# Kernel tuning notes

Hardware: AMD Instinct MI355X
Metric: run time of the kernel (lower is better)

## Reference

```python
import jax, jax.numpy as jnp
import numpy as np

HIDDEN = 2048
NUM_HEADS = 16
HEAD_SIZE = HIDDEN // NUM_HEADS  # 128
SEQ = 2048
BATCH = 2


def alibi_causal_bias(seq_len: int, num_heads: int) -> jnp.ndarray:
    """[1, H, S, S] bias: -(i-j)*slope for j<=i, -inf for j>i (per source mask)."""
    i = jnp.arange(seq_len)[:, None]
    j = jnp.arange(seq_len)[None, :]
    dist = -(i - j).astype(jnp.float32)            # 0 on diag, -(i-j) below
    causal = jnp.where(j > i, -jnp.inf, 0.0)
    base = jnp.where(j > i, 0.0, dist) + causal     # [S, S]
    if num_heads <= 8:
        slopes = jnp.asarray([1.0 / 2**k for k in range(num_heads)], jnp.float32)
    else:
        slopes = jnp.asarray([1.0 / 2**(k / 2) for k in range(num_heads)], jnp.float32)
    # NOTE: source multiplies the mask (including -inf part) by the slope;
    # -inf * positive slope is still -inf, so applying slopes to the finite
    # part and adding -inf causal term is equivalent.
    return slopes[None, :, None, None] * dist[None, None] * (j <= i)[None, None] + causal[None, None]


def setup_inputs() -> dict:
    key = jax.random.key(0)
    ks = jax.random.split(key, 3)
    sd = 1.0 / np.sqrt(HIDDEN)
    return {
        "x": jax.random.normal(ks[0], (BATCH, SEQ, HIDDEN), jnp.float32),
        "Wqkv": jax.random.normal(ks[1], (HIDDEN, 3 * HIDDEN), jnp.float32) * sd,
        "bqkv": jnp.zeros((3 * HIDDEN,), jnp.float32),
        "Wo": jax.random.normal(ks[2], (HIDDEN, HIDDEN), jnp.float32) * sd,
        "bo": jnp.zeros((HIDDEN,), jnp.float32),
    }


def reference(x, Wqkv, bqkv, Wo, bo):
    b, s, h = x.shape
    scale = 1.0 / np.sqrt(HEAD_SIZE)
    qkv = x @ Wqkv + bqkv                                   # [b, s, 3h]
    q, k, v = jnp.split(qkv, 3, axis=-1)
    def heads(t):
        return t.reshape(b, s, NUM_HEADS, HEAD_SIZE).transpose(0, 2, 1, 3)
    q, k, v = heads(q), heads(k), heads(v)                  # [b, H, s, d]
    scores = jnp.einsum("bhid,bhjd->bhij", q, k) * scale
    scores = scores + alibi_causal_bias(s, NUM_HEADS)
    attn = jax.nn.softmax(scores, axis=-1)                  # dropout=0 (eval)
    out = jnp.einsum("bhij,bhjd->bhid", attn, v)            # [b, H, s, d]
    out = out.transpose(0, 2, 1, 3).reshape(b, s, NUM_HEADS * HEAD_SIZE)
    return out @ Wo + bo
```

## Files before the change

### kernel.cpp

```cpp
#include <hip/hip_runtime.h>

typedef __attribute__((ext_vector_type(4))) float f32x4;
typedef __attribute__((ext_vector_type(8))) __bf16 bf16x8;
typedef unsigned short u16;

#define GAS(p) ((const __attribute__((address_space(1))) void*)(p))
#define LAS(p) ((__attribute__((address_space(3))) void*)(p))

__device__ __forceinline__ u16 f32_to_bf16(float f) {
  unsigned u = __builtin_bit_cast(unsigned, f);
  u += 0x7FFFu + ((u >> 16) & 1u);
  return (u16)(u >> 16);
}

__global__ __launch_bounds__(256) void k_convert(const float* __restrict__ X,
                                                 u16* __restrict__ Y, int n4) {
  int i = blockIdx.x * 256 + threadIdx.x;
  if (i >= n4) return;
  float4 v = ((const float4*)X)[i];
  ushort4 r;
  r.x = f32_to_bf16(v.x); r.y = f32_to_bf16(v.y);
  r.z = f32_to_bf16(v.z); r.w = f32_to_bf16(v.w);
  ((ushort4*)Y)[i] = r;
}

__global__ __launch_bounds__(256) void k_transpose_w(const float* __restrict__ W,
                                                     u16* __restrict__ WT,
                                                     int K, int N) {
  __shared__ float tile[32][33];
  int n0 = blockIdx.x * 32, k0 = blockIdx.y * 32;
  int tx = threadIdx.x & 31, ty = threadIdx.x >> 5;
#pragma unroll
  for (int r = 0; r < 4; ++r)
    tile[ty + r * 8][tx] = W[(long)(k0 + ty + r * 8) * N + n0 + tx];
  __syncthreads();
#pragma unroll
  for (int r = 0; r < 4; ++r)
    WT[(long)(n0 + ty + r * 8) * K + k0 + tx] = f32_to_bf16(tile[tx][ty + r * 8]);
}

__global__ __launch_bounds__(256) void k_transpose_v(const u16* __restrict__ V,
                                                     u16* __restrict__ VT) {
  __shared__ u16 tile[32][34];
  int s0 = blockIdx.x * 32, d0 = blockIdx.y * 32, bh = blockIdx.z;
  int tx = threadIdx.x & 31, ty = threadIdx.x >> 5;
  const u16* Vb = V + (long)bh * 2048 * 128;
  u16* VTb = VT + (long)bh * 128 * 2048;
#pragma unroll
  for (int r = 0; r < 4; ++r)
    tile[ty + r * 8][tx] = Vb[(long)(s0 + ty + r * 8) * 128 + d0 + tx];
  __syncthreads();
#pragma unroll
  for (int r = 0; r < 4; ++r)
    VTb[(long)(d0 + ty + r * 8) * 2048 + s0 + tx] = tile[tx][ty + r * 8];
}

template <int EPI>
__global__ __launch_bounds__(256) void k_gemm(
    const u16* __restrict__ A, const u16* __restrict__ BT,
    const float* __restrict__ bias,
    u16* __restrict__ Qo, u16* __restrict__ Ko, u16* __restrict__ Vo,
    float* __restrict__ Cout, int M, int N, int K) {
  __shared__ alignas(16) u16 As[128 * 32];
  __shared__ alignas(16) u16 Bs[128 * 32];
  const int t = threadIdx.x;
  const int wave = t >> 6, lane = t & 63;
  const int wr = wave >> 1, wc = wave & 1;
  const int l15 = lane & 15, l4 = lane >> 4;
  const int brow = blockIdx.x * 128, bcol = blockIdx.y * 128;

  const f32x4 fzero = {0.f, 0.f, 0.f, 0.f};
  f32x4 acc[4][4];
#pragma unroll
  for (int m = 0; m < 4; ++m)
#pragma unroll
    for (int n = 0; n < 4; ++n) acc[m][n] = fzero;

  const int c0 = wave * 64 + lane;
  const int c1 = 256 + c0;
  const u16* ga0 = A + (long)(brow + (c0 >> 2)) * K + (c0 & 3) * 8;
  const u16* ga1 = A + (long)(brow + (c1 >> 2)) * K + (c1 & 3) * 8;
  const u16* gb0 = BT + (long)(bcol + (c0 >> 2)) * K + (c0 & 3) * 8;
  const u16* gb1 = BT + (long)(bcol + (c1 >> 2)) * K + (c1 & 3) * 8;
  char* lA0 = (char*)As + (wave * 64) * 16;
  char* lA1 = (char*)As + (256 + wave * 64) * 16;
  char* lB0 = (char*)Bs + (wave * 64) * 16;
  char* lB1 = (char*)Bs + (256 + wave * 64) * 16;

  for (int k0 = 0; k0 < K; k0 += 32) {
    __builtin_amdgcn_global_load_lds(GAS(ga0 + k0), LAS(lA0), 16, 0, 0);
    __builtin_amdgcn_global_load_lds(GAS(ga1 + k0), LAS(lA1), 16, 0, 0);
    __builtin_amdgcn_global_load_lds(GAS(gb0 + k0), LAS(lB0), 16, 0, 0);
    __builtin_amdgcn_global_load_lds(GAS(gb1 + k0), LAS(lB1), 16, 0, 0);
    __syncthreads();
    bf16x8 af[4], bf[4];
#pragma unroll
    for (int m = 0; m < 4; ++m)
      af[m] = *(const bf16x8*)(As + (wr * 64 + m * 16 + l15) * 32 + l4 * 8);
#pragma unroll
    for (int n = 0; n < 4; ++n)
      bf[n] = *(const bf16x8*)(Bs + (wc * 64 + n * 16 + l15) * 32 + l4 * 8);
#pragma unroll
    for (int m = 0; m < 4; ++m)
#pragma unroll
      for (int n = 0; n < 4; ++n)
        acc[m][n] =
            __builtin_amdgcn_mfma_f32_16x16x32_bf16(af[m], bf[n], acc[m][n], 0, 0, 0);
    __syncthreads();
  }

  if (EPI == 0) {
    const int which = bcol >> 11;
    u16* dst = (which == 0) ? Qo : (which == 1) ? Ko : Vo;
    const int cbase = bcol & 2047;
#pragma unroll
    for (int n = 0; n < 4; ++n) {
      int col = cbase + wc * 64 + n * 16 + l15;
      int h = col >> 7, d = col & 127;
      float bv = bias[bcol + wc * 64 + n * 16 + l15];
#pragma unroll
      for (int m = 0; m < 4; ++m) {
#pragma unroll
        for (int r = 0; r < 4; ++r) {
          int row = brow + wr * 64 + m * 16 + l4 * 4 + r;
          int b = row >> 11, s = row & 2047;
          dst[(((long)(b * 16 + h)) * 2048 + s) * 128 + d] =
              f32_to_bf16(acc[m][n][r] + bv);
        }
      }
    }
  } else {
#pragma unroll
    for (int m = 0; m < 4; ++m) {
#pragma unroll
      for (int r = 0; r < 4; ++r) {
        int row = brow + wr * 64 + m * 16 + l4 * 4 + r;
#pragma unroll
        for (int n = 0; n < 4; ++n) {
          int col = bcol + wc * 64 + n * 16 + l15;
          Cout[(long)row * N + col] = acc[m][n][r] + bias[col];
        }
      }
    }
  }
}

__global__ __launch_bounds__(256, 4) void k_attn(const u16* __restrict__ Q,
                                                 const u16* __restrict__ Kp,
                                                 const u16* __restrict__ VT,
                                                 u16* __restrict__ Oa) {
  __shared__ alignas(16) u16 Kl[2][64 * 128];
  __shared__ alignas(16) u16 Vl[2][128 * 64];
  __shared__ alignas(16) u16 Pl[4][16 * 64];
  const int b = blockIdx.x;
  const int bh = b & 31;
  const int qt = 31 - (b >> 5);
  const int bb = bh >> 4, h = bh & 15;
  const int wave = threadIdx.x >> 6, lane = threadIdx.x & 63;
  const int l15 = lane & 15, l4 = lane >> 4;
  const int l7 = lane & 7, l8 = lane >> 3;
  const float LOG2E = 1.4426950408889634f;
  const float scale = 0.08838834764831845f * LOG2E;
  const float slope = exp2f(-0.5f * (float)h) * LOG2E;

  const int q0 = qt * 64 + wave * 16;
  const u16* Qb = Q + ((long)bh * 2048 + q0 + l15) * 128;
  bf16x8 qf[4];
#pragma unroll
  for (int kk = 0; kk < 4; ++kk) qf[kk] = *(const bf16x8*)(Qb + kk * 32 + l4 * 8);

  const u16* Kb = Kp + (long)bh * 2048 * 128;
  const u16* VTb = VT + (long)bh * 128 * 2048;

  auto stageK = [&](int jt, int buf) {
#pragma unroll
    for (int g = 0; g < 4; ++g) {
      const int wc = g * 4 + wave;
      const int row = wc * 4 + l4;
      const u16* src = Kb + (long)(jt * 64 + row) * 128 + ((l15 ^ (row & 7)) * 8);
      __builtin_amdgcn_global_load_lds(GAS(src), LAS(&Kl[buf][wc * 512]), 16, 0, 0);
    }
  };
  auto stageV = [&](int jt, int buf) {
#pragma unroll
    for (int g = 0; g < 4; ++g) {
      const int wc = g * 4 + wave;
      const int d = wc * 8 + l8;
      const u16* src = VTb + (long)d * 2048 + jt * 64 + ((l7 ^ l8) * 8);
      __builtin_amdgcn_global_load_lds(GAS(src), LAS(&Vl[buf][wc * 512]), 16, 0, 0);
    }
  };

  float rs[4];
  f32x4 O[8];
  const f32x4 fzero = {0.f, 0.f, 0.f, 0.f};
#pragma unroll
  for (int r = 0; r < 4; ++r) rs[r] = 0.f;
#pragma unroll
  for (int nb = 0; nb < 8; ++nb) O[nb] = fzero;

  u16* Pw = Pl[wave];
  const int irow = q0 + l4 * 4;
  const int sw = l15 & 7;

  stageK(0, 0);
  stageV(0, 0);
  __syncthreads();

  for (int jt = 0; jt <= qt; ++jt) {
    const int cur = jt & 1;
    if (jt < qt) {
      stageK(jt + 1, cur ^ 1);
      stageV(jt + 1, cur ^ 1);
    }
    const u16* Kc = Kl[cur];
    const u16* Vc = Vl[cur];
    const int j0 = jt * 64;
#pragma unroll
    for (int cb = 0; cb < 4; ++cb) {
      f32x4 sa = fzero;
      const u16* kp = Kc + (cb * 16 + l15) * 128;
#pragma unroll
      for (int kk = 0; kk < 4; ++kk) {
        bf16x8 kf = *(const bf16x8*)(kp + (((kk * 4 + l4) ^ sw) * 8));
        sa = __builtin_amdgcn_mfma_f32_16x16x32_bf16(qf[kk], kf, sa, 0, 0, 0);
      }
      const int j = j0 + cb * 16 + l15;
#pragma unroll
      for (int r = 0; r < 4; ++r) {
        int i = irow + r;
        float s = sa[r] * scale - slope * (float)(i - j);
        float p = __builtin_amdgcn_exp2f((j <= i) ? s : -1e30f);
        rs[r] += p;
        int rloc = l4 * 4 + r;
        int cbyte = (cb * 16 + l15) * 2;
        *(u16*)((char*)Pw + rloc * 128 + (cbyte ^ ((rloc & 7) << 4))) =
            f32_to_bf16(p);
      }
    }
    bf16x8 pf0 = *(const bf16x8*)((char*)Pw + l15 * 128 +
                                  ((l4 * 16) ^ ((l15 & 7) << 4)));
    bf16x8 pf1 = *(const bf16x8*)((char*)Pw + l15 * 128 +
                                  ((64 + l4 * 16) ^ ((l15 & 7) << 4)));
#pragma unroll
    for (int nb = 0; nb < 8; ++nb) {
      const u16* vp = Vc + (nb * 16 + l15) * 64;
      bf16x8 v0 = *(const bf16x8*)(vp + ((l4 ^ sw) * 8));
      bf16x8 v1 = *(const bf16x8*)(vp + (((4 + l4) ^ sw) * 8));
      O[nb] = __builtin_amdgcn_mfma_f32_16x16x32_bf16(pf0, v0, O[nb], 0, 0, 0);
      O[nb] = __builtin_amdgcn_mfma_f32_16x16x32_bf16(pf1, v1, O[nb], 0, 0, 0);
    }
    __syncthreads();
  }
#pragma unroll
  for (int r = 0; r < 4; ++r) {
    float v = rs[r];
    v += __shfl_xor(v, 1);
    v += __shfl_xor(v, 2);
    v += __shfl_xor(v, 4);
    v += __shfl_xor(v, 8);
    float inv = 1.f / v;
    int i = irow + r;
    u16* op = Oa + ((long)bb * 2048 + i) * 2048 + h * 128;
#pragma unroll
    for (int nb = 0; nb < 8; ++nb) op[nb * 16 + l15] = f32_to_bf16(O[nb][r] * inv);
  }
}

extern "C" void kernel_launch(void* const* d_in, const int* in_sizes, int n_in,
                              void* d_out, int out_size, void* d_ws, size_t ws_size,
                              hipStream_t stream) {
  const float* x = (const float*)d_in[0];
  const float* Wqkv = (const float*)d_in[1];
  const float* bqkv = (const float*)d_in[2];
  const float* Wo = (const float*)d_in[3];
  const float* bo = (const float*)d_in[4];
  float* out = (float*)d_out;

  char* ws = (char*)d_ws;
  u16* xb = (u16*)(ws);
  u16* VTb = (u16*)(ws);
  u16* WqkvT = (u16*)(ws + 16777216);
  u16* attn_out = (u16*)(ws + 16777216);
  u16* WoT = (u16*)(ws + 16777216 + 25165824);
  u16* Qb = (u16*)(ws + 50331648);
  u16* Kb = (u16*)(ws + 67108864);
  u16* Vb = (u16*)(ws + 83886080);

  k_convert<<<8192, 256, 0, stream>>>(x, xb, 8388608 / 4);
  k_transpose_w<<<dim3(192, 64), 256, 0, stream>>>(Wqkv, WqkvT, 2048, 6144);
  k_transpose_w<<<dim3(64, 64), 256, 0, stream>>>(Wo, WoT, 2048, 2048);
  k_gemm<0><<<dim3(32, 48), 256, 0, stream>>>(xb, WqkvT, bqkv, Qb, Kb, Vb,
                                              nullptr, 4096, 6144, 2048);
  k_transpose_v<<<dim3(64, 4, 32), 256, 0, stream>>>(Vb, VTb);
  k_attn<<<dim3(1024), 256, 0, stream>>>(Qb, Kb, VTb, attn_out);
  k_gemm<1><<<dim3(32, 16), 256, 0, stream>>>(attn_out, WoT, bo, nullptr,
                                              nullptr, nullptr, out, 4096, 2048,
                                              2048);
}
```

Measured before the change: 289.4 us.

## Rewrite GEMM with 256x128 tiles, triple-buffered LDS pipeline, swizzled loads and grid remap

Restructures the bf16 GEMM used for the QKV and output projections. Each block now has 512 threads and computes a 256x128 tile with K-steps of 64. Loads go into a triple-buffered LDS ring that prefetches two steps ahead and waits on partial vmcnt, and LDS addresses are XOR-swizzled to avoid bank conflicts. The grid is remapped so that neighbouring blocks share A or B tiles in L2, and s_setprio raises priority around the MFMA bursts. The goal is to hide global-load latency and cut the barrier and LDS overhead of the old single-buffer 128x128x32 loop, at the cost of much more LDS per block (about 144 KB) and lower occupancy.

After: 284.6 us. Within noise of the previous version (-1.6%).

```diff
diff --git a/kernel.cpp b/kernel.cpp
--- a/kernel.cpp
+++ b/kernel.cpp
@@ -56,92 +56,143 @@
 }
 
 template <int EPI>
-__global__ __launch_bounds__(256) void k_gemm(
+__global__ __launch_bounds__(512, 2) void k_gemm(
     const u16* __restrict__ A, const u16* __restrict__ BT,
     const float* __restrict__ bias,
     u16* __restrict__ Qo, u16* __restrict__ Ko, u16* __restrict__ Vo,
     float* __restrict__ Cout, int M, int N, int K) {
-  __shared__ alignas(16) u16 As[128 * 32];
-  __shared__ alignas(16) u16 Bs[128 * 32];
-  const int t = threadIdx.x;
-  const int wave = t >> 6, lane = t & 63;
-  const int wr = wave >> 1, wc = wave & 1;
+  __shared__ alignas(16) u16 AS[3][256 * 64];
+  __shared__ alignas(16) u16 BS[3][128 * 64];
+  const int wave = threadIdx.x >> 6, lane = threadIdx.x & 63;
+  const int wr = wave >> 2, wc = wave & 3;
   const int l15 = lane & 15, l4 = lane >> 4;
-  const int brow = blockIdx.x * 128, bcol = blockIdx.y * 128;
+  const int sl = lane & 7, sr = (lane >> 3) & 7;
+
+  const int nwg = gridDim.x;
+  const int swz = ((int)blockIdx.x & 7) * (nwg >> 3) + ((int)blockIdx.x >> 3);
+  const int mt = M >> 8;
+  const int bm = swz % mt, bn = swz / mt;
+  const int brow = bm * 256, bcol = bn * 128;
+  const int NT = K >> 6;
+
+  const u16* aSrc[4];
+  const u16* bSrc[2];
+#pragma unroll
+  for (int j = 0; j < 4; ++j) {
+    int row = (wave + j * 8) * 8 + (lane >> 3);
+    aSrc[j] = A + (long)(brow + row) * K + ((sl ^ sr) * 8);
+  }
+#pragma unroll
+  for (int j = 0; j < 2; ++j) {
+    int row = (wave + j * 8) * 8 + (lane >> 3);
+    bSrc[j] = BT + (long)(bcol + row) * K + ((sl ^ sr) * 8);
+  }
+
+  auto stage = [&](int t, int buf) {
+#pragma unroll
+    for (int j = 0; j < 4; ++j)
+      __builtin_amdgcn_global_load_lds(GAS(aSrc[j] + t * 64),
+                                       LAS(&AS[buf][(wave + j * 8) * 512]), 16, 0, 0);
+#pragma unroll
+    for (int j = 0; j < 2; ++j)
+      __builtin_amdgcn_global_load_lds(GAS(bSrc[j] + t * 64),
+                                       LAS(&BS[buf][(wave + j * 8) * 512]), 16, 0, 0);
+  };
 
   const f32x4 fzero = {0.f, 0.f, 0.f, 0.f};
-  f32x4 acc[4][4];
-#pragma unroll
-  for (int m = 0; m < 4; ++m)
-#pragma unroll
-    for (int n = 0; n < 4; ++n) acc[m][n] = fzero;
-
-  const int c0 = wave * 64 + lane;
-  const int c1 = 256 + c0;
-  const u16* ga0 = A + (long)(brow + (c0 >> 2)) * K + (c0 & 3) * 8;
-  const u16* ga1 = A + (long)(brow + (c1 >> 2)) * K + (c1 & 3) * 8;
-  const u16* gb0 = BT + (long)(bcol + (c0 >> 2)) * K + (c0 & 3) * 8;
-  const u16* gb1 = BT + (long)(bcol + (c1 >> 2)) * K + (c1 & 3) * 8;
-  char* lA0 = (char*)As + (wave * 64) * 16;
-  char* lA1 = (char*)As + (256 + wave * 64) * 16;
-  char* lB0 = (char*)Bs + (wave * 64) * 16;
-  char* lB1 = (char*)Bs + (256 + wave * 64) * 16;
-
-  for (int k0 = 0; k0 < K; k0 += 32) {
-    __builtin_amdgcn_global_load_lds(GAS(ga0 + k0), LAS(lA0), 16, 0, 0);
-    __builtin_amdgcn_global_load_lds(GAS(ga1 + k0), LAS(lA1), 16, 0, 0);
-    __builtin_amdgcn_global_load_lds(GAS(gb0 + k0), LAS(lB0), 16, 0, 0);
-    __builtin_amdgcn_global_load_lds(GAS(gb1 + k0), LAS(lB1), 16, 0, 0);
-    __syncthreads();
-    bf16x8 af[4], bf[4];
-#pragma unroll
-    for (int m = 0; m < 4; ++m)
-      af[m] = *(const bf16x8*)(As + (wr * 64 + m * 16 + l15) * 32 + l4 * 8);
-#pragma unroll
-    for (int n = 0; n < 4; ++n)
-      bf[n] = *(const bf16x8*)(Bs + (wc * 64 + n * 16 + l15) * 32 + l4 * 8);
-#pragma unroll
-    for (int m = 0; m < 4; ++m)
-#pragma unroll
-      for (int n = 0; n < 4; ++n)
-        acc[m][n] =
-            __builtin_amdgcn_mfma_f32_16x16x32_bf16(af[m], bf[n], acc[m][n], 0, 0, 0);
-    __syncthreads();
-  }
+  f32x4 acc[8][2];
+#pragma unroll
+  for (int m = 0; m < 8; ++m)
+#pragma unroll
+    for (int n = 0; n < 2; ++n) acc[m][n] = fzero;
+
+  auto compute = [&](int buf) {
+    const u16* Ac = &AS[buf][0];
+    const u16* Bc = &BS[buf][0];
+    bf16x8 bfr[2][2];
+#pragma unroll
+    for (int n = 0; n < 2; ++n)
+#pragma unroll
+      for (int kk = 0; kk < 2; ++kk) {
+        int R = wc * 32 + n * 16 + l15;
+        bfr[n][kk] =
+            *(const bf16x8*)(Bc + R * 64 + (((kk * 4 + l4) ^ (l15 & 7)) * 8));
+      }
+#pragma unroll
+    for (int mh = 0; mh < 2; ++mh) {
+      bf16x8 afr[4][2];
+#pragma unroll
+      for (int mm = 0; mm < 4; ++mm)
+#pragma unroll
+        for (int kk = 0; kk < 2; ++kk) {
+          int R = wr * 128 + (mh * 4 + mm) * 16 + l15;
+          afr[mm][kk] =
+              *(const bf16x8*)(Ac + R * 64 + (((kk * 4 + l4) ^ (l15 & 7)) * 8));
+        }
+      __builtin_amdgcn_s_setprio(1);
+#pragma unroll
+      for (int mm = 0; mm < 4; ++mm)
+#pragma unroll
+        for (int n = 0; n < 2; ++n)
+#pragma unroll
+          for (int kk = 0; kk < 2; ++kk)
+            acc[mh * 4 + mm][n] = __builtin_amdgcn_mfma_f32_16x16x32_bf16(
+                afr[mm][kk], bfr[n][kk], acc[mh * 4 + mm][n], 0, 0, 0);
+      __builtin_amdgcn_s_setprio(0);
+    }
+  };
+
+  stage(0, 0);
+  stage(1, 1);
+  int bufc = 0;
+  for (int t = 0; t < NT - 1; ++t) {
+    asm volatile("s_waitcnt vmcnt(6)" ::: "memory");
+    __builtin_amdgcn_s_barrier();
+    if (t + 2 < NT) {
+      int bufn = bufc + 2;
+      if (bufn >= 3) bufn -= 3;
+      stage(t + 2, bufn);
+    }
+    compute(bufc);
+    ++bufc;
+    if (bufc == 3) bufc = 0;
+  }
+  asm volatile("s_waitcnt vmcnt(0)" ::: "memory");
+  __builtin_amdgcn_s_barrier();
+  compute(bufc);
 
   if (EPI == 0) {
-    const int which = bcol >> 11;
-    u16* dst = (which == 0) ? Qo : (which == 1) ? Ko : Vo;
-    const int cbase = bcol & 2047;
-#pragma unroll
-    for (int n = 0; n < 4; ++n) {
-      int col = cbase + wc * 64 + n * 16 + l15;
-      int h = col >> 7, d = col & 127;
-      float bv = bias[bcol + wc * 64 + n * 16 + l15];
-#pragma unroll
-      for (int m = 0; m < 4; ++m) {
+#pragma unroll
+    for (int n = 0; n < 2; ++n) {
+      const int col = bcol + wc * 32 + n * 16 + l15;
+      const int which = col >> 11;
+      u16* dst = (which == 0) ? Qo : (which == 1) ? Ko : Vo;
+      const int cc = col & 2047;
+      const int h = cc >> 7, d = cc & 127;
+      const float bv = bias[col];
+#pragma unroll
+      for (int m = 0; m < 8; ++m) {
 #pragma unroll
         for (int r = 0; r < 4; ++r) {
-          int row = brow + wr * 64 + m * 16 + l4 * 4 + r;
-          int b = row >> 11, s = row & 2047;
-          dst[(((long)(b * 16 + h)) * 2048 + s) * 128 + d] =
+          const int row = brow + wr * 128 + m * 16 + l4 * 4 + r;
+          const int bb = row >> 11, s = row & 2047;
+          dst[(((long)(bb * 16 + h)) * 2048 + s) * 128 + d] =
               f32_to_bf16(acc[m][n][r] + bv);
         }
       }
     }
   } else {
 #pragma unroll
-    for (int m = 0; m < 4; ++m) {
+    for (int m = 0; m < 8; ++m)
 #pragma unroll
       for (int r = 0; r < 4; ++r) {
-        int row = brow + wr * 64 + m * 16 + l4 * 4 + r;
-#pragma unroll
-        for (int n = 0; n < 4; ++n) {
-          int col = bcol + wc * 64 + n * 16 + l15;
+        const int row = brow + wr * 128 + m * 16 + l4 * 4 + r;
+#pragma unroll
+        for (int n = 0; n < 2; ++n) {
+          const int col = bcol + wc * 32 + n * 16 + l15;
           Cout[(long)row * N + col] = acc[m][n][r] + bias[col];
         }
       }
-    }
   }
 }
 
@@ -175,19 +226,19 @@
   auto stageK = [&](int jt, int buf) {
 #pragma unroll
     for (int g = 0; g < 4; ++g) {
-      const int wc = g * 4 + wave;
-      const int row = wc * 4 + l4;
+      const int wcc = g * 4 + wave;
+      const int row = wcc * 4 + l4;
       const u16* src = Kb + (long)(jt * 64 + row) * 128 + ((l15 ^ (row & 7)) * 8);
-      __builtin_amdgcn_global_load_lds(GAS(src), LAS(&Kl[buf][wc * 512]), 16, 0, 0);
+      __builtin_amdgcn_global_load_lds(GAS(src), LAS(&Kl[buf][wcc * 512]), 16, 0, 0);
     }
   };
   auto stageV = [&](int jt, int buf) {
 #pragma unroll
     for (int g = 0; g < 4; ++g) {
-      const int wc = g * 4 + wave;
-      const int d = wc * 8 + l8;
+      const int wcc = g * 4 + wave;
+      const int d = wcc * 8 + l8;
       const u16* src = VTb + (long)d * 2048 + jt * 64 + ((l7 ^ l8) * 8);
-      __builtin_amdgcn_global_load_lds(GAS(src), LAS(&Vl[buf][wc * 512]), 16, 0, 0);
+      __builtin_amdgcn_global_load_lds(GAS(src), LAS(&Vl[buf][wcc * 512]), 16, 0, 0);
     }
   };
 
@@ -290,11 +341,11 @@
   k_convert<<<8192, 256, 0, stream>>>(x, xb, 8388608 / 4);
   k_transpose_w<<<dim3(192, 64), 256, 0, stream>>>(Wqkv, WqkvT, 2048, 6144);
   k_transpose_w<<<dim3(64, 64), 256, 0, stream>>>(Wo, WoT, 2048, 2048);
-  k_gemm<0><<<dim3(32, 48), 256, 0, stream>>>(xb, WqkvT, bqkv, Qb, Kb, Vb,
-                                              nullptr, 4096, 6144, 2048);
+  k_gemm<0><<<dim3(768), 512, 0, stream>>>(xb, WqkvT, bqkv, Qb, Kb, Vb,
+                                           nullptr, 4096, 6144, 2048);
   k_transpose_v<<<dim3(64, 4, 32), 256, 0, stream>>>(Vb, VTb);
   k_attn<<<dim3(1024), 256, 0, stream>>>(Qb, Kb, VTb, attn_out);
-  k_gemm<1><<<dim3(32, 16), 256, 0, stream>>>(attn_out, WoT, bo, nullptr,
-                                              nullptr, nullptr, out, 4096, 2048,
-                                              2048);
-}
+  k_gemm<1><<<dim3(256), 512, 0, stream>>>(attn_out, WoT, bo, nullptr,
+                                           nullptr, nullptr, out, 4096, 2048,
+                                           2048);
+}
```
